# Kernel tuning notes

Hardware: AMD Instinct MI355X
Metric: run time of the kernel (lower is better)

## Reference

```python
import jax, jax.numpy as jnp
import numpy as np

B, S, D = 2, 2048, 2048
H, KVH, HD = 16, 8, 128
EPS = 1e-6
ROPE_THETA = 10000.0


def _rope_cache(seq_len, head_dim):
    inv_freq = 1.0 / (ROPE_THETA ** (np.arange(0, head_dim, 2, dtype=np.float32) / head_dim))
    t = np.arange(seq_len, dtype=np.float32)
    freqs = np.outer(t, inv_freq)                      # [S, HD/2]
    emb = np.concatenate([freqs, freqs], axis=-1)      # [S, HD]
    return jnp.asarray(np.cos(emb)), jnp.asarray(np.sin(emb))


def setup_inputs() -> dict:
    key = jax.random.key(0)
    ks = jax.random.split(key, 10)
    x = jax.random.normal(ks[0], (B, S, D), dtype=jnp.float32)
    wq_q = jax.random.randint(ks[1], (H * HD, D), -127, 128, dtype=jnp.int32)
    wk_q = jax.random.randint(ks[2], (KVH * HD, D), -127, 128, dtype=jnp.int32)
    wv_q = jax.random.randint(ks[3], (KVH * HD, D), -127, 128, dtype=jnp.int32)
    wo_q = jax.random.randint(ks[4], (D, H * HD), -127, 128, dtype=jnp.int32)
    # per-output-channel scales (realistic small magnitudes)
    wq_s = jax.random.uniform(ks[5], (H * HD,), minval=1e-3, maxval=2e-2)
    wk_s = jax.random.uniform(ks[6], (KVH * HD,), minval=1e-3, maxval=2e-2)
    wv_s = jax.random.uniform(ks[7], (KVH * HD,), minval=1e-3, maxval=2e-2)
    wo_s = jax.random.uniform(ks[8], (D,), minval=1e-3, maxval=2e-2)
    q_norm_w = jnp.ones((HD,), dtype=jnp.float32)
    k_norm_w = jnp.ones((HD,), dtype=jnp.float32)
    cos_cache, sin_cache = _rope_cache(S, HD)
    return {"x": x, "wq_q": wq_q, "wq_s": wq_s, "wk_q": wk_q, "wk_s": wk_s,
            "wv_q": wv_q, "wv_s": wv_s, "wo_q": wo_q, "wo_s": wo_s,
            "q_norm_w": q_norm_w, "k_norm_w": k_norm_w,
            "cos_cache": cos_cache, "sin_cache": sin_cache}


def _dequant_linear(x, wq, ws):
    # W8A16-style: dequantize int8 weight with per-channel scale, then GEMM
    w = wq.astype(jnp.float32) * ws[:, None]   # [out, in]
    return x @ w.T


def _rms_norm(x, w, eps=EPS):
    var = jnp.mean(x * x, axis=-1, keepdims=True)
    return x * jax.lax.rsqrt(var + eps) * w


def _rotate_half(x):
    x1, x2 = jnp.split(x, 2, axis=-1)
    return jnp.concatenate([-x2, x1], axis=-1)


def _apply_rope(q, k, cos, sin):
    # q: [B,S,H,HD], k: [B,S,KVH,HD]; cos/sin: [S,HD] -> broadcast over batch, heads
    cos = cos[None, :, None, :]
    sin = sin[None, :, None, :]
    q = q * cos + _rotate_half(q) * sin
    k = k * cos + _rotate_half(k) * sin
    return q, k


def reference(x, wq_q, wq_s, wk_q, wk_s, wv_q, wv_s, wo_q, wo_s,
              q_norm_w, k_norm_w, cos_cache, sin_cache):
    batch, seq_len, dim = x.shape
    q = _dequant_linear(x, wq_q, wq_s).reshape(batch, seq_len, H, HD)
    k = _dequant_linear(x, wk_q, wk_s).reshape(batch, seq_len, KVH, HD)
    v = _dequant_linear(x, wv_q, wv_s).reshape(batch, seq_len, KVH, HD)
    q = _rms_norm(q, q_norm_w)
    k = _rms_norm(k, k_norm_w)
    # first forward: cache is empty -> kv = current k,v
    q, k = _apply_rope(q, k, cos_cache[:seq_len], sin_cache[:seq_len])
    q = q.transpose(0, 2, 1, 3)   # [B,H,S,HD]
    k = k.transpose(0, 2, 1, 3)   # [B,KVH,S,HD]
    v = v.transpose(0, 2, 1, 3)
    rep = H // KVH
    k = jnp.repeat(k, rep, axis=1)  # GQA repeat_interleave -> [B,H,S,HD]
    v = jnp.repeat(v, rep, axis=1)
    scale = 1.0 / jnp.sqrt(jnp.asarray(HD, dtype=x.dtype))
    scores = jnp.einsum('bhqd,bhkd->bhqk', q, k) * scale
    causal = jnp.tril(jnp.ones((seq_len, seq_len), dtype=bool))
    scores = jnp.where(causal[None, None], scores, jnp.finfo(scores.dtype).min)
    attn = jax.nn.softmax(scores, axis=-1)
    out = jnp.einsum('bhqk,bhkd->bhqd', attn, v)
    out = out.transpose(0, 2, 1, 3).reshape(batch, seq_len, H * HD)
    return _dequant_linear(out, wo_q, wo_s)
```

## Files before the change

kernel.cpp:

```cpp
#include <hip/hip_runtime.h>


typedef __attribute__((ext_vector_type(4))) float floatx4;
typedef __attribute__((ext_vector_type(8))) short short8v;
typedef __attribute__((ext_vector_type(4))) short short4v;
typedef __attribute__((ext_vector_type(8))) unsigned short ushort8v;

#define DEVINL __device__ __forceinline__

constexpr int cB = 2, cS = 2048, cD = 2048, cH = 16, cKVH = 8, cHD = 128;
constexpr int cM = cB * cS;
constexpr int cNqkv = (cH + 2 * cKVH) * cHD;
constexpr float cEPS = 1e-6f;
constexpr float cSCL2 = 0.08838834764831845f * 1.4426950408889634f;

DEVINL unsigned short f2bf(float f) {
  unsigned u = __float_as_uint(f);
  unsigned r = ((u >> 16) & 1u) + 0x7FFFu;
  return (unsigned short)((u + r) >> 16);
}
DEVINL float bf2f(unsigned short h) { return __uint_as_float(((unsigned)h) << 16); }

DEVINL floatx4 mfma_bf16(short8v a, short8v b, floatx4 c) {
  return __builtin_amdgcn_mfma_f32_16x16x32_bf16(a, b, c, 0, 0, 0);
}

DEVINL void gl_lds16(const void* g, void* l) {
  __builtin_amdgcn_global_load_lds(
      (const __attribute__((address_space(1))) void*)g,
      (__attribute__((address_space(3))) void*)l, 16, 0, 0);
}

__global__ void detect_dtype(const unsigned* __restrict__ x, int* __restrict__ flag) {
  __shared__ int cnt;
  if (threadIdx.x == 0) cnt = 0;
  __syncthreads();
  int c = 0;
  for (int i = threadIdx.x; i < 4096; i += 256) {
    unsigned e = (x[i] >> 7) & 0xFFu;
    c += (e >= 100u && e <= 142u) ? 1 : 0;
  }
  atomicAdd(&cnt, c);
  __syncthreads();
  if (threadIdx.x == 0) *flag = (cnt > 2457) ? 1 : 0;
}

__global__ void conv_small(const void* p9, const void* p10, const void* p2,
                           const void* p4, const void* p6, const void* p8,
                           float* __restrict__ nw, float* __restrict__ scat,
                           float* __restrict__ so, const int* __restrict__ flag) {
  int i = blockIdx.x * 256 + threadIdx.x;
  int f = *flag;
  auto rd = [&](const void* p, int idx) -> float {
    return f ? bf2f(((const unsigned short*)p)[idx]) : ((const float*)p)[idx];
  };
  if (i < 256) {
    nw[i] = (i < 128) ? rd(p9, i) : rd(p10, i - 128);
  } else if (i < 256 + 4096) {
    int j = i - 256;
    scat[j] = (j < 2048) ? rd(p2, j) : (j < 3072 ? rd(p4, j - 2048) : rd(p6, j - 3072));
  } else if (i < 256 + 4096 + 2048) {
    int j = i - 4352;
    so[j] = rd(p8, j);
  }
}

__global__ void rope_pack(const void* __restrict__ cosc, const void* __restrict__ sinc,
                          float2* __restrict__ tab, const int* __restrict__ flag) {
  int i = blockIdx.x * 256 + threadIdx.x;
  if (i >= cS * 64) return;
  int s = i >> 6, t = i & 63;
  int f = *flag;
  float c = f ? bf2f(((const unsigned short*)cosc)[s * cHD + t])
              : ((const float*)cosc)[s * cHD + t];
  float sn = f ? bf2f(((const unsigned short*)sinc)[s * cHD + t])
               : ((const float*)sinc)[s * cHD + t];
  tab[i] = make_float2(c, sn);
}

DEVINL void pack_body(const void* src, unsigned short* dst, int K, int md,
                      int Trow, int Tdst, int kc, int tid, float L[16][264]) {
#pragma unroll
  for (int it = 0; it < 16; it++) {
    int e = it * 256 + tid;
    int r = e >> 8, c = e & 255;
    size_t idx = (size_t)(Trow * 16 + r) * K + kc * 256 + c;
    float v;
    if (md == 1)      v = ((const float*)src)[idx];
    else if (md == 2) v = (float)((const int*)src)[idx];
    else              v = bf2f(((const unsigned short*)src)[idx]);
    L[r][c] = v;
  }
  __syncthreads();
  const int lane = tid & 63, w = tid >> 6;
  const int q = lane >> 4, l16 = lane & 15;
#pragma unroll
  for (int p = 0; p < 2; p++) {
    int kbl = w + p * 4;
    ushort8v o;
#pragma unroll
    for (int j = 0; j < 8; j++) o[j] = f2bf(L[l16][kbl * 32 + q * 8 + j]);
    *(ushort8v*)(dst + ((size_t)Tdst * 64 + kc * 8 + kbl) * 512 + lane * 8) = o;
  }
}

__global__ __launch_bounds__(256) void pack_frag(
    const void* __restrict__ src, unsigned short* __restrict__ dst,
    int K, int mode, const int* __restrict__ flag) {
  __shared__ float L[16][264];
  int md = mode;
  if (md == 0) md = (*flag) ? 3 : 1;
  pack_body(src, dst, K, md, blockIdx.x, blockIdx.x, blockIdx.y, threadIdx.x, L);
}

__global__ __launch_bounds__(256) void pack_wqkv(
    const int* __restrict__ wq, const int* __restrict__ wk,
    const int* __restrict__ wv, unsigned short* __restrict__ dst) {
  __shared__ float L[16][264];
  int T = blockIdx.x;
  const int* src;
  int Trow;
  if (T < 128)      { src = wq; Trow = T; }
  else if (T < 192) { src = wk; Trow = T - 128; }
  else              { src = wv; Trow = T - 192; }
  pack_body(src, dst, 2048, 2, Trow, T, blockIdx.y, threadIdx.x, L);
}

DEVINL void gemm_core4(const unsigned short* __restrict__ Ap,
                       const unsigned short* __restrict__ Bp,
                       int tm0, int tn0, int nkb, int lane,
                       floatx4 acc[4][4]) {
  const unsigned short* ap[4];
  const unsigned short* bp[4];
#pragma unroll
  for (int i = 0; i < 4; i++) {
    ap[i] = Ap + ((size_t)(tm0 + i) * 64) * 512 + lane * 8;
    bp[i] = Bp + ((size_t)(tn0 + i) * 64) * 512 + lane * 8;
  }
  short8v a[4][4], b[4][4];
#pragma unroll
  for (int p = 0; p < 4; p++)
#pragma unroll
    for (int i = 0; i < 4; i++) {
      a[p][i] = *(const short8v*)(ap[i] + p * 512);
      b[p][i] = *(const short8v*)(bp[i] + p * 512);
    }
  for (int kb = 0; kb < nkb; kb += 4) {
    const bool more = (kb + 4) < nkb;
#pragma unroll
    for (int p = 0; p < 4; p++) {
#pragma unroll
      for (int mt = 0; mt < 4; mt++)
#pragma unroll
        for (int nt = 0; nt < 4; nt++)
          acc[mt][nt] = mfma_bf16(a[p][mt], b[p][nt], acc[mt][nt]);
      if (more) {
        const int o = (kb + 4 + p) * 512;
#pragma unroll
        for (int i = 0; i < 4; i++) {
          a[p][i] = *(const short8v*)(ap[i] + o);
          b[p][i] = *(const short8v*)(bp[i] + o);
        }
      }
    }
  }
}

__global__ __launch_bounds__(256) void gemm_qkv(
    const unsigned short* __restrict__ Ap, const unsigned short* __restrict__ Bp,
    const float* __restrict__ colscale, const float2* __restrict__ ropetab,
    const float* __restrict__ nw, unsigned short* __restrict__ Qb,
    unsigned short* __restrict__ Kb, unsigned short* __restrict__ Vt) {
  __shared__ float4 smem4[2192];
  char* smem = (char*)smem4;
  const int tid = threadIdx.x;
  const int lane = tid & 63, wave = tid >> 6;
  const int q = lane >> 4, l16 = lane & 15;
  const int m0 = blockIdx.y * 128, n0 = blockIdx.x * 128;
  const int wm = (wave & 1) * 64, wn = (wave >> 1) * 64;

  floatx4 acc[4][4] = {};
  gemm_core4(Ap, Bp, (m0 + wm) >> 4, (n0 + wn) >> 4, cD / 32, lane, acc);

  float sc[4];
#pragma unroll
  for (int nt = 0; nt < 4; nt++) sc[nt] = colscale[n0 + wn + nt * 16 + l16];
#pragma unroll
  for (int mt = 0; mt < 4; mt++)
#pragma unroll
    for (int nt = 0; nt < 4; nt++)
#pragma unroll
      for (int rg = 0; rg < 4; rg++) acc[mt][nt][rg] *= sc[nt];

  const int tile_n = blockIdx.x;
  const int bi = m0 >> 11, sbase = m0 & (cS - 1);

  if (tile_n >= 24) {
    unsigned short* T = (unsigned short*)smem;
#pragma unroll
    for (int mt = 0; mt < 4; mt++)
#pragma unroll
      for (int nt = 0; nt < 4; nt++) {
        short4v pk;
#pragma unroll
        for (int rg = 0; rg < 4; rg++) pk[rg] = (short)f2bf(acc[mt][nt][rg]);
        *(short4v*)(T + (wn + nt * 16 + l16) * 136 + (wm + mt * 16 + q * 4)) = pk;
      }
    __syncthreads();
    const int d = tid >> 1, sh = (tid & 1) * 64;
    unsigned short* dst = Vt + ((size_t)(bi * cKVH + (tile_n - 24)) * cHD + d) * cS
                          + sbase + sh;
#pragma unroll
    for (int j = 0; j < 8; j++)
      *(ushort8v*)(dst + j * 8) = *(const ushort8v*)(T + d * 136 + sh + j * 8);
  } else {
    unsigned short* W = (unsigned short*)smem;
    float* ssq  = (float*)(smem + 32768);
    float* invs = (float*)(smem + 33792);

    float sl[4][4];
#pragma unroll
    for (int mt = 0; mt < 4; mt++)
#pragma unroll
      for (int rg = 0; rg < 4; rg++) {
        float s = 0.f;
#pragma unroll
        for (int nt = 0; nt < 4; nt++) s += acc[mt][nt][rg] * acc[mt][nt][rg];
        s += __shfl_xor(s, 1); s += __shfl_xor(s, 2);
        s += __shfl_xor(s, 4); s += __shfl_xor(s, 8);
        sl[mt][rg] = s;
      }
    unsigned short* Wo = W + wave * 4096;
#pragma unroll
    for (int mt = 0; mt < 4; mt++)
#pragma unroll
      for (int nt = 0; nt < 4; nt++) {
        short4v pk;
#pragma unroll
        for (int rg = 0; rg < 4; rg++) pk[rg] = (short)f2bf(acc[mt][nt][rg]);
        *(short4v*)(Wo + (mt * 4 + nt) * 256 + lane * 4) = pk;
      }
    if (l16 == 0) {
#pragma unroll
      for (int mt = 0; mt < 4; mt++)
#pragma unroll
        for (int rg = 0; rg < 4; rg++)
          ssq[((wave >> 1) & 1) * 128 + wm + mt * 16 + q * 4 + rg] = sl[mt][rg];
    }
    __syncthreads();
    if (tid < 128)
      invs[tid] = rsqrtf((ssq[tid] + ssq[128 + tid]) * (1.0f / cHD) + cEPS);
    __syncthreads();

    const unsigned short* Wp = W + (wave ^ 2) * 4096;
    const int wn1 = wave >> 1;
    const float* nwb = nw + (tile_n < 16 ? 0 : cHD);
    float wown[4], wpar[4];
#pragma unroll
    for (int nt = 0; nt < 4; nt++) {
      wown[nt] = nwb[wn1 * 64 + nt * 16 + l16];
      wpar[nt] = nwb[(wn1 ^ 1) * 64 + nt * 16 + l16];
    }
    unsigned short* dstb = (tile_n < 16)
        ? Qb + ((size_t)(bi * cH + tile_n) * cS) * cHD
        : Kb + ((size_t)(bi * cKVH + (tile_n - 16)) * cS) * cHD;
#pragma unroll
    for (int mt = 0; mt < 4; mt++) {
      float iv[4];
#pragma unroll
      for (int rg = 0; rg < 4; rg++) iv[rg] = invs[wm + mt * 16 + q * 4 + rg];
#pragma unroll
      for (int nt = 0; nt < 4; nt++) {
        short4v pk = *(const short4v*)(Wp + (mt * 4 + nt) * 256 + lane * 4);
#pragma unroll
        for (int rg = 0; rg < 4; rg++) {
          int srow = sbase + wm + mt * 16 + q * 4 + rg;
          float2 cs = ropetab[srow * 64 + nt * 16 + l16];
          float nown = acc[mt][nt][rg] * iv[rg] * wown[nt];
          float npar = bf2f((unsigned short)pk[rg]) * iv[rg] * wpar[nt];
          float o = wn1 == 0 ? nown * cs.x - npar * cs.y
                             : nown * cs.x + npar * cs.y;
          dstb[(size_t)srow * cHD + wn1 * 64 + nt * 16 + l16] = f2bf(o);
        }
      }
    }
  }
}

__global__ __launch_bounds__(256) void gemm_out(
    const unsigned short* __restrict__ Ap, const unsigned short* __restrict__ Bp,
    const float* __restrict__ colscale, void* __restrict__ Cout,
    const int* __restrict__ flag, int N, int nkb) {
  const int tid = threadIdx.x;
  const int lane = tid & 63, wave = tid >> 6;
  const int q = lane >> 4, l16 = lane & 15;
  const int m0 = blockIdx.y * 128, n0 = blockIdx.x * 128;
  const int wm = (wave & 1) * 64, wn = (wave >> 1) * 64;

  floatx4 acc[4][4] = {};
  gemm_core4(Ap, Bp, (m0 + wm) >> 4, (n0 + wn) >> 4, nkb, lane, acc);

  const int f = *flag;
#pragma unroll
  for (int mt = 0; mt < 4; mt++) {
    int r0 = m0 + wm + mt * 16 + q * 4;
#pragma unroll
    for (int nt = 0; nt < 4; nt++) {
      int cn = n0 + wn + nt * 16 + l16;
      float sc = colscale[cn];
#pragma unroll
      for (int rg = 0; rg < 4; rg++) {
        float v = acc[mt][nt][rg] * sc;
        if (f) ((unsigned short*)Cout)[(size_t)(r0 + rg) * N + cn] = f2bf(v);
        else   ((float*)Cout)[(size_t)(r0 + rg) * N + cn] = v;
      }
    }
  }
}

__global__ __launch_bounds__(256, 4) void attn(
    const unsigned short* __restrict__ Qb, const unsigned short* __restrict__ Kb,
    const unsigned short* __restrict__ Vt, unsigned short* __restrict__ AOp) {
  __shared__ unsigned short SM[16384];
  const int tid = threadIdx.x;
  const int lane = tid & 63, wv = tid >> 6;
  const int q = lane >> 4, l16 = lane & 15;
  const int bi = blockIdx.z, h = blockIdx.y;
  const int kh = h >> 1;
  const int bx = (int)blockIdx.x;
  const int qt = (bx & 1) ? (31 - (bx >> 1)) : (bx >> 1);
  const int q0 = qt * 64;
  const int q0w = q0 + wv * 16;

  const unsigned short* Qbase = Qb + ((size_t)(bi * cH + h) * cS + q0w) * cHD;
  const unsigned short* Kbase = Kb + ((size_t)(bi * cKVH + kh) * cS) * cHD;
  const unsigned short* Vbase = Vt + ((size_t)(bi * cKVH + kh) * cHD) * cS;

  short8v qa[4];
#pragma unroll
  for (int c = 0; c < 4; c++)
    qa[c] = *(const short8v*)(Qbase + (size_t)l16 * cHD + c * 32 + q * 8);

  floatx4 oacc[8] = {};
  float lp = 0.f;

  int koff[2];
#pragma unroll
  for (int i = 0; i < 2; i++) {
    int s = (wv * 2 + i) * 64 + lane;
    int r = s >> 4, u = (s & 15) ^ (r & 15);
    int sig = ((r >> 2) & 3) * 8 + ((r >> 4) & 1) * 4 + (r & 3);
    koff[i] = sig * cHD + u * 8;
  }
  int voff[2];
#pragma unroll
  for (int i = 0; i < 2; i++) {
    int s = (wv * 2 + i) * 64 + lane;
    int d = s >> 2, c2 = (s & 3) ^ (d & 3);
    voff[i] = d * cS + c2 * 8;
  }

  const int nwin = 2 * qt + 2;
  auto stage = [&](int win) {
    const int buf = (win & 1) * 8192;
    const int kv0 = win * 32;
    unsigned short* Kdst = SM + buf + (wv * 2) * 512;
    unsigned short* Vdst = SM + buf + 4096 + (wv * 2) * 512;
#pragma unroll
    for (int i = 0; i < 2; i++)
      gl_lds16(Kbase + (size_t)kv0 * cHD + koff[i], Kdst + i * 512);
#pragma unroll
    for (int i = 0; i < 2; i++)
      gl_lds16(Vbase + (size_t)kv0 + voff[i], Vdst + i * 512);
  };

  stage(0);
  for (int win = 0; win < nwin; win++) {
    __syncthreads();
    if (win + 1 < nwin) stage(win + 1);
    const int kv0 = win * 32;
    if (kv0 <= q0w + 15) {
      const unsigned short* Ks = SM + (win & 1) * 8192;
      const unsigned short* Vs = Ks + 4096;

      floatx4 sres[2] = {};
#pragma unroll
      for (int c = 0; c < 4; c++) {
        short8v kf[2];
#pragma unroll
        for (int ntk = 0; ntk < 2; ntk++)
          kf[ntk] = *(const short8v*)(Ks + (ntk * 16 + l16) * 128 +
                                      (((c * 4 + q) ^ l16) * 8));
#pragma unroll
        for (int ntk = 0; ntk < 2; ntk++)
          sres[ntk] = mfma_bf16(kf[ntk], qa[c], sres[ntk]);
      }

      const bool maskw = (kv0 + 31 > q0w);
      short8v pa8;
#pragma unroll
      for (int ntk = 0; ntk < 2; ntk++) {
#pragma unroll
        for (int rg = 0; rg < 4; rg++) {
          float e = exp2f(sres[ntk][rg] * cSCL2);
          if (maskw) {
            int kvloc = q * 8 + ntk * 4 + rg;
            if (kv0 + kvloc > q0w + l16) e = 0.f;
          }
          lp += e;
          pa8[ntk * 4 + rg] = (short)f2bf(e);
        }
      }

#pragma unroll
      for (int db = 0; db < 8; db++) {
        short8v vb = *(const short8v*)(Vs + (db * 16 + l16) * 32 +
                                       ((q ^ (l16 & 3)) * 8));
        oacc[db] = mfma_bf16(pa8, vb, oacc[db]);
      }
    }
  }

  float lf = lp;
  lf += __shfl_xor(lf, 16);
  lf += __shfl_xor(lf, 32);
  float li[4];
#pragma unroll
  for (int rg = 0; rg < 4; rg++) li[rg] = 1.0f / __shfl(lf, q * 4 + rg);

  __syncthreads();
  unsigned short* T = SM + wv * 16 * 136;
#pragma unroll
  for (int rg = 0; rg < 4; rg++)
#pragma unroll
    for (int db = 0; db < 8; db++)
      T[(q * 4 + rg) * 136 + db * 16 + l16] = f2bf(oacc[db][rg] * li[rg]);
  const int mtile = (bi * cS + q0w) >> 4;
#pragma unroll
  for (int kbl = 0; kbl < 4; kbl++) {
    short8v fr = *(const short8v*)(T + l16 * 136 + kbl * 32 + q * 8);
    *(short8v*)(AOp + ((size_t)mtile * 64 + h * 4 + kbl) * 512 + lane * 8) = fr;
  }
}

extern "C" void kernel_launch(void* const* d_in, const int* in_sizes, int n_in,
                              void* d_out, int out_size, void* d_ws, size_t ws_size,
                              hipStream_t stream) {
  (void)in_sizes; (void)n_in; (void)out_size; (void)ws_size;
  char* ws = (char*)d_ws;
  size_t off = 0;
  auto alloc = [&](size_t bytes) -> char* {
    char* p = ws + off;
    off += (bytes + 255) & ~((size_t)255);
    return p;
  };
  int* flag            = (int*)alloc(256);
  float2* ropetab      = (float2*)alloc((size_t)cS * 64 * 8);
  float* nw            = (float*)alloc(256 * 4);
  float* scat          = (float*)alloc(4096 * 4);
  float* so            = (float*)alloc(2048 * 4);
  unsigned short* xp   = (unsigned short*)alloc((size_t)cM * cD * 2);
  unsigned short* wp   = (unsigned short*)alloc((size_t)cNqkv * cD * 2);
  unsigned short* wop  = (unsigned short*)alloc((size_t)cD * cH * cHD * 2);
  unsigned short* Qb   = (unsigned short*)alloc((size_t)cB * cH * cS * cHD * 2);
  unsigned short* Kb   = (unsigned short*)alloc((size_t)cB * cKVH * cS * cHD * 2);
  unsigned short* Vt   = (unsigned short*)alloc((size_t)cB * cKVH * cHD * cS * 2);
  unsigned short* AOp  = (unsigned short*)alloc((size_t)cM * cD * 2);

  detect_dtype<<<1, 256, 0, stream>>>((const unsigned*)d_in[0], flag);
  conv_small<<<25, 256, 0, stream>>>(d_in[9], d_in[10], d_in[2], d_in[4], d_in[6],
                                     d_in[8], nw, scat, so, flag);
  rope_pack<<<(cS * 64 + 255) / 256, 256, 0, stream>>>(d_in[11], d_in[12], ropetab, flag);
  pack_frag<<<dim3(256, 8), 256, 0, stream>>>(d_in[0], xp, 2048, 0, flag);
  pack_wqkv<<<dim3(256, 8), 256, 0, stream>>>((const int*)d_in[1], (const int*)d_in[3],
                                              (const int*)d_in[5], wp);
  pack_frag<<<dim3(128, 8), 256, 0, stream>>>(d_in[7], wop, 2048, 2, flag);

  gemm_qkv<<<dim3(cNqkv / 128, cM / 128), 256, 0, stream>>>(
      xp, wp, scat, ropetab, nw, Qb, Kb, Vt);
  attn<<<dim3(cS / 64, cH, cB), 256, 0, stream>>>(Qb, Kb, Vt, AOp);
  gemm_out<<<dim3(cD / 128, cM / 128), 256, 0, stream>>>(
      AOp, wop, so, d_out, flag, cD, (cH * cHD) / 32);
}
```

Measured before the change: 410.2 us.

## Stage GEMM tiles through double-buffered LDS and remap blocks per XCD

Replaces the register-only GEMM core, where every wave loaded its own A and B fragments straight from global memory, with a cooperative double-buffered LDS staging scheme. Each k-step the four waves jointly copy the block's 8 A and 8 B tiles into shared memory with gl_lds16 and then read their fragments from LDS. This cuts redundant global traffic, since each tile was previously fetched by two waves. Both GEMM kernels also remap block IDs so that blocks landing on the same XCD share N-tiles, to improve L2 locality. The cost is a __syncthreads per k-step and less register-level prefetch depth.

```diff
diff --git a/kernel.cpp b/kernel.cpp
--- a/kernel.cpp
+++ b/kernel.cpp
@@ -126,43 +126,45 @@
   pack_body(src, dst, 2048, 2, Trow, T, blockIdx.y, threadIdx.x, L);
 }
 
-DEVINL void gemm_core4(const unsigned short* __restrict__ Ap,
-                       const unsigned short* __restrict__ Bp,
-                       int tm0, int tn0, int nkb, int lane,
-                       floatx4 acc[4][4]) {
-  const unsigned short* ap[4];
-  const unsigned short* bp[4];
+DEVINL void gemm_core(const unsigned short* __restrict__ Ap,
+                      const unsigned short* __restrict__ Bp,
+                      unsigned short* __restrict__ SM,
+                      int tmB, int tnB, int nkb, int tid,
+                      floatx4 acc[4][4]) {
+  const int lane = tid & 63, wv = tid >> 6;
+  const unsigned short* g[4];
 #pragma unroll
   for (int i = 0; i < 4; i++) {
-    ap[i] = Ap + ((size_t)(tm0 + i) * 64) * 512 + lane * 8;
-    bp[i] = Bp + ((size_t)(tn0 + i) * 64) * 512 + lane * 8;
-  }
-  short8v a[4][4], b[4][4];
-#pragma unroll
-  for (int p = 0; p < 4; p++)
-#pragma unroll
-    for (int i = 0; i < 4; i++) {
-      a[p][i] = *(const short8v*)(ap[i] + p * 512);
-      b[p][i] = *(const short8v*)(bp[i] + p * 512);
-    }
-  for (int kb = 0; kb < nkb; kb += 4) {
-    const bool more = (kb + 4) < nkb;
-#pragma unroll
-    for (int p = 0; p < 4; p++) {
-#pragma unroll
-      for (int mt = 0; mt < 4; mt++)
-#pragma unroll
-        for (int nt = 0; nt < 4; nt++)
-          acc[mt][nt] = mfma_bf16(a[p][mt], b[p][nt], acc[mt][nt]);
-      if (more) {
-        const int o = (kb + 4 + p) * 512;
-#pragma unroll
-        for (int i = 0; i < 4; i++) {
-          a[p][i] = *(const short8v*)(ap[i] + o);
-          b[p][i] = *(const short8v*)(bp[i] + o);
-        }
-      }
-    }
+    int t = i * 4 + wv;
+    g[i] = (t < 8 ? Ap + ((size_t)(tmB + t) * 64) * 512
+                  : Bp + ((size_t)(tnB + t - 8) * 64) * 512) + lane * 8;
+  }
+  const int at0 = (wv & 1) * 4, bt0 = 8 + (wv >> 1) * 4;
+
+  auto stage = [&](int kb) {
+    unsigned short* buf = SM + (kb & 1) * 8192;
+#pragma unroll
+    for (int i = 0; i < 4; i++)
+      gl_lds16(g[i] + (size_t)kb * 512, buf + (i * 4 + wv) * 512 + lane * 8);
+  };
+
+  stage(0);
+  for (int kb = 0; kb < nkb; kb++) {
+    __syncthreads();
+    if (kb + 1 < nkb) stage(kb + 1);
+    const unsigned short* buf = SM + (kb & 1) * 8192;
+    short8v a[4], b[4];
+#pragma unroll
+    for (int mt = 0; mt < 4; mt++)
+      a[mt] = *(const short8v*)(buf + (at0 + mt) * 512 + lane * 8);
+#pragma unroll
+    for (int nt = 0; nt < 4; nt++)
+      b[nt] = *(const short8v*)(buf + (bt0 + nt) * 512 + lane * 8);
+#pragma unroll
+    for (int mt = 0; mt < 4; mt++)
+#pragma unroll
+      for (int nt = 0; nt < 4; nt++)
+        acc[mt][nt] = mfma_bf16(a[mt], b[nt], acc[mt][nt]);
   }
 }
 
@@ -176,11 +178,14 @@
   const int tid = threadIdx.x;
   const int lane = tid & 63, wave = tid >> 6;
   const int q = lane >> 4, l16 = lane & 15;
-  const int m0 = blockIdx.y * 128, n0 = blockIdx.x * 128;
+  const int wg = (int)blockIdx.y * 32 + (int)blockIdx.x;
+  const int xcd = wg & 7, cix = wg >> 3;
+  const int bxn = (xcd << 2) | (cix & 3), byn = cix >> 2;
+  const int m0 = byn * 128, n0 = bxn * 128;
   const int wm = (wave & 1) * 64, wn = (wave >> 1) * 64;
 
   floatx4 acc[4][4] = {};
-  gemm_core4(Ap, Bp, (m0 + wm) >> 4, (n0 + wn) >> 4, cD / 32, lane, acc);
+  gemm_core(Ap, Bp, (unsigned short*)smem, m0 >> 4, n0 >> 4, cD / 32, tid, acc);
 
   float sc[4];
 #pragma unroll
@@ -192,7 +197,8 @@
 #pragma unroll
       for (int rg = 0; rg < 4; rg++) acc[mt][nt][rg] *= sc[nt];
 
-  const int tile_n = blockIdx.x;
+  __syncthreads();
+  const int tile_n = bxn;
   const int bi = m0 >> 11, sbase = m0 & (cS - 1);
 
   if (tile_n >= 24) {
@@ -291,14 +297,18 @@
     const unsigned short* __restrict__ Ap, const unsigned short* __restrict__ Bp,
     const float* __restrict__ colscale, void* __restrict__ Cout,
     const int* __restrict__ flag, int N, int nkb) {
+  __shared__ unsigned short SM[16384];
   const int tid = threadIdx.x;
   const int lane = tid & 63, wave = tid >> 6;
   const int q = lane >> 4, l16 = lane & 15;
-  const int m0 = blockIdx.y * 128, n0 = blockIdx.x * 128;
+  const int wg = (int)blockIdx.y * 16 + (int)blockIdx.x;
+  const int xcd = wg & 7, cix = wg >> 3;
+  const int bxn = (xcd << 1) | (cix & 1), byn = cix >> 1;
+  const int m0 = byn * 128, n0 = bxn * 128;
   const int wm = (wave & 1) * 64, wn = (wave >> 1) * 64;
 
   floatx4 acc[4][4] = {};
-  gemm_core4(Ap, Bp, (m0 + wm) >> 4, (n0 + wn) >> 4, nkb, lane, acc);
+  gemm_core(Ap, Bp, SM, m0 >> 4, n0 >> 4, nkb, tid, acc);
 
   const int f = *flag;
 #pragma unroll
```

After: 442.3 us. 7.8% more time.
